# Optimization experiments

Measured on AMD Instinct MI355X. Metric: run time of the kernel, lower is better.

The kernel has to match this reference:

```python
import jax, jax.numpy as jnp
import numpy as np

N = 50000      # nodes
E = 800000     # edges
IN = 128       # in_channels
H = 256        # hidden_channels
EMB = 128      # embedding_size
R = 4          # num_relations
HEADS = 2


def setup_inputs() -> dict:
    key = jax.random.key(0)
    ks = jax.random.split(key, 20)
    w = lambda k, shape: jax.random.normal(k, shape, dtype=jnp.float32) * 0.05
    return dict(
        x=jax.random.normal(ks[0], (N, IN), dtype=jnp.float32),
        edge_index=jax.random.randint(ks[1], (2, E), 0, N, dtype=jnp.int32),
        edge_type=jax.random.randint(ks[2], (E,), 0, R, dtype=jnp.int32),
        sage1_Wl=w(ks[3], (IN, H)), sage1_Wr=w(ks[4], (IN, H)), sage1_b=jnp.zeros((H,), jnp.float32),
        sage2_Wl=w(ks[5], (H, H)), sage2_Wr=w(ks[6], (H, H)), sage2_b=jnp.zeros((H,), jnp.float32),
        gat_W=w(ks[7], (H, HEADS * H)), gat_att_src=w(ks[8], (HEADS, H)), gat_att_dst=w(ks[9], (HEADS, H)),
        gat_b=jnp.zeros((H,), jnp.float32),
        rgcn_Wrel=w(ks[10], (R, H, EMB)), rgcn_Wroot=w(ks[11], (H, EMB)), rgcn_b=jnp.zeros((EMB,), jnp.float32),
        fusion_W=w(ks[12], (H + H + EMB, EMB)), fusion_b=jnp.zeros((EMB,), jnp.float32),
    )


def _segmean(msg, seg, num_segments):
    s = jax.ops.segment_sum(msg, seg, num_segments=num_segments)
    c = jax.ops.segment_sum(jnp.ones((seg.shape[0], 1), msg.dtype), seg, num_segments=num_segments)
    return s / jnp.maximum(c, 1.0)


def _sage(x, src, dst, Wl, Wr, b, n):
    # SAGEConv: lin_l(mean_j x_j) + lin_r(x_i)
    agg = _segmean(x[src], dst, n)
    return agg @ Wl + x @ Wr + b


def _gat(x, src, dst, W, a_src, a_dst, b, n):
    # GATConv heads=2, concat=False (head average), add_self_loops=True
    loop = jnp.arange(n, dtype=src.dtype)
    src = jnp.concatenate([src, loop])
    dst = jnp.concatenate([dst, loop])
    h = (x @ W).reshape(n, HEADS, -1)                 # [N, heads, H]
    al_src = (h * a_src).sum(-1)                      # [N, heads]
    al_dst = (h * a_dst).sum(-1)                      # [N, heads]
    e = jax.nn.leaky_relu(al_src[src] + al_dst[dst], 0.2)   # [E', heads]
    m = jax.ops.segment_max(e, dst, num_segments=n)          # stable softmax per dst node
    ex = jnp.exp(e - m[dst])
    den = jax.ops.segment_sum(ex, dst, num_segments=n)
    alpha = ex / jnp.maximum(den[dst], 1e-16)
    out = jax.ops.segment_sum(alpha[:, :, None] * h[src], dst, num_segments=n)  # [N, heads, H]
    return out.mean(axis=1) + b


def _rgcn(x, src, dst, etype, Wrel, Wroot, b, n, r):
    # RGCNConv: sum_r mean_{j in N_r(i)} W_r x_j + W_root x_i + b
    xt = jnp.einsum('nh,rhe->rne', x, Wrel)           # [R, N, EMB]
    m = xt[etype, src]                                # [E, EMB]
    seg = dst * r + etype                             # per (node, relation) segment
    agg = _segmean(m, seg, n * r).reshape(n, r, -1).sum(axis=1)
    return agg + x @ Wroot + b


def reference(x, edge_index, edge_type,
              sage1_Wl, sage1_Wr, sage1_b,
              sage2_Wl, sage2_Wr, sage2_b,
              gat_W, gat_att_src, gat_att_dst, gat_b,
              rgcn_Wrel, rgcn_Wroot, rgcn_b,
              fusion_W, fusion_b):
    src, dst = edge_index[0], edge_index[1]
    n = x.shape[0]
    x1 = jax.nn.relu(_sage(x, src, dst, sage1_Wl, sage1_Wr, sage1_b, n))
    # dropout(p=0.2) is identity in eval mode
    x_sage = jax.nn.relu(_sage(x1, src, dst, sage2_Wl, sage2_Wr, sage2_b, n))
    x_gat = jax.nn.relu(_gat(x_sage, src, dst, gat_W, gat_att_src, gat_att_dst, gat_b, n))
    x_rgcn = _rgcn(x_gat, src, dst, edge_type, rgcn_Wrel, rgcn_Wroot, rgcn_b, n, R)
    x_all = jnp.concatenate([x_sage, x_gat, x_rgcn], axis=1)
    out = x_all @ fusion_W + fusion_b
    norm = jnp.maximum(jnp.linalg.norm(out, axis=1, keepdims=True), 1e-12)
    return out / norm
```

## Files before the change

kernel.cpp:

```cpp
#include <hip/hip_runtime.h>
#include <hip/hip_fp16.h>
#include <math.h>

constexpr int NN   = 50000;
constexpr int NE   = 800000;
constexpr int NREL = 4;
constexpr int NB   = (NN + 255) / 256;

typedef _Float16 half8 __attribute__((ext_vector_type(8)));
typedef __attribute__((ext_vector_type(4))) float floatx4;

__device__ inline unsigned short f16_rne(float x) {
  return __half_as_ushort(__float2half_rn(x));
}
__device__ inline float h2f(unsigned short h) {
  return __half2float(__ushort_as_half(h));
}

__global__ void k_counts(const int* __restrict__ dst, const int* __restrict__ et,
                         int* cntrel) {
  int e = blockIdx.x * blockDim.x + threadIdx.x;
  if (e < NE) {
    int d = dst[e];
    atomicAdd(&cntrel[d * NREL + et[e]], 1);
  }
}

__global__ void k_scan1(const int* __restrict__ cntrel, int* bsum) {
  __shared__ int sm[256];
  int i = blockIdx.x * 256 + threadIdx.x;
  int v = 0;
  if (i < NN) { int4 c = ((const int4*)cntrel)[i]; v = c.x + c.y + c.z + c.w; }
  sm[threadIdx.x] = v;
  __syncthreads();
  for (int s = 128; s; s >>= 1) {
    if (threadIdx.x < s) sm[threadIdx.x] += sm[threadIdx.x + s];
    __syncthreads();
  }
  if (threadIdx.x == 0) bsum[blockIdx.x] = sm[0];
}
__global__ void k_scan2(const int* __restrict__ bsum, int* boff, int* rowptr) {
  if (threadIdx.x == 0 && blockIdx.x == 0) {
    int acc = 0;
    for (int b = 0; b < NB; ++b) { boff[b] = acc; acc += bsum[b]; }
    rowptr[NN] = NE;
  }
}
__global__ void k_scan3(const int* __restrict__ cntrel, const int* __restrict__ boff,
                        int* rowptr) {
  __shared__ int sm[256];
  int i = blockIdx.x * 256 + threadIdx.x;
  int v = 0;
  if (i < NN) { int4 c = ((const int4*)cntrel)[i]; v = c.x + c.y + c.z + c.w; }
  sm[threadIdx.x] = v;
  __syncthreads();
  for (int s = 1; s < 256; s <<= 1) {
    int t = (threadIdx.x >= s) ? sm[threadIdx.x - s] : 0;
    __syncthreads();
    sm[threadIdx.x] += t;
    __syncthreads();
  }
  if (i < NN) rowptr[i] = boff[blockIdx.x] + sm[threadIdx.x] - v;
}

__global__ void k_fill(const int* __restrict__ src, const int* __restrict__ dst,
                       const int* __restrict__ et, const int* __restrict__ rowptr,
                       int* cursor, int* srcs, int* ets) {
  int e = blockIdx.x * blockDim.x + threadIdx.x;
  if (e >= NE) return;
  int d = dst[e];
  int pos = rowptr[d] + atomicAdd(&cursor[d], 1);
  srcs[pos] = src[e];
  ets[pos]  = et[e];
}

#define PK_N 14
__device__ __constant__ const int PK_BASE[PK_N]  = {0,1,2,3,4,4,5,5,5,5,6,7,7,7};
__device__ __constant__ const int PK_EOFF[PK_N]  = {0,0,0,0,0,256,0,32768,65536,98304,0,0,32768,65536};
__device__ __constant__ const int PK_K[PK_N]     = {128,128,256,256,256,256,256,256,256,256,256,256,256,128};
__device__ __constant__ const int PK_LDB[PK_N]   = {256,256,256,256,512,512,128,128,128,128,128,128,128,128};
__device__ __constant__ const int PK_START[PK_N] = {0,4096,8192,16384,24576,32768,40960,45056,49152,53248,57344,61440,65536,69632};
constexpr int PK_TOTAL = 71680;
constexpr int BF_S1WL = 0,     BF_S1WR = 4096,  BF_S2WL = 8192,  BF_S2WR = 16384;
constexpr int BF_GATW0 = 24576, BF_GATW1 = 32768, BF_WREL = 40960, BF_WROOT = 57344;
constexpr int BF_FW0 = 61440,  BF_FW1 = 65536,  BF_FW2 = 69632;

__global__ void k_pack(const float* b0, const float* b1, const float* b2, const float* b3,
                       const float* b4, const float* b5, const float* b6, const float* b7,
                       unsigned short* __restrict__ Bh) {
  int f = blockIdx.x * 256 + threadIdx.x;
  if (f >= PK_TOTAL) return;
  int m = 0;
#pragma unroll
  for (int i = 1; i < PK_N; ++i) if (f >= PK_START[i]) m = i;
  const float* bases[8] = {b0,b1,b2,b3,b4,b5,b6,b7};
  int lf = f - PK_START[m];
  int K = PK_K[m], ldb = PK_LDB[m];
  int Kq16 = K << 1;
  int ntile = lf / Kq16;
  int rem = lf - ntile * Kq16;
  int kq = rem >> 4, c = rem & 15;
  const float* sp = bases[PK_BASE[m]] + PK_EOFF[m] + (size_t)(kq * 8) * ldb + ntile * 16 + c;
#pragma unroll
  for (int j = 0; j < 8; ++j)
    Bh[(size_t)f * 8 + j] = f16_rne(sp[(size_t)j * ldb]);
}

__global__ void k_split(const float* __restrict__ x, unsigned short* __restrict__ xh,
                        long total4) {
  long i = (long)blockIdx.x * blockDim.x + threadIdx.x;
  if (i >= total4) return;
  float4 v = ((const float4*)x)[i];
  ushort4 h;
  h.x = f16_rne(v.x); h.y = f16_rne(v.y);
  h.z = f16_rne(v.z); h.w = f16_rne(v.w);
  ((ushort4*)xh)[i] = h;
}

__global__ void k_mean128p(const unsigned short* __restrict__ ih, const int* __restrict__ rowptr,
                           const int* __restrict__ srcs,
                           unsigned short* __restrict__ oh) {
  int node = blockIdx.x * 4 + (threadIdx.x >> 6);
  int lane = threadIdx.x & 63;
  if (node >= NN) return;
  int p0 = rowptr[node], p1 = rowptr[node + 1];
  float2 acc = make_float2(0.f, 0.f);
  int p = p0;
  for (; p + 4 <= p1; p += 4) {
    int s0 = srcs[p], s1 = srcs[p+1], s2 = srcs[p+2], s3 = srcs[p+3];
    ushort2 v0 = ((const ushort2*)(ih + ((size_t)s0 << 7)))[lane];
    ushort2 v1 = ((const ushort2*)(ih + ((size_t)s1 << 7)))[lane];
    ushort2 v2 = ((const ushort2*)(ih + ((size_t)s2 << 7)))[lane];
    ushort2 v3 = ((const ushort2*)(ih + ((size_t)s3 << 7)))[lane];
    acc.x += (h2f(v0.x) + h2f(v1.x)) + (h2f(v2.x) + h2f(v3.x));
    acc.y += (h2f(v0.y) + h2f(v1.y)) + (h2f(v2.y) + h2f(v3.y));
  }
  for (; p < p1; ++p) {
    int s = srcs[p];
    ushort2 hv = ((const ushort2*)(ih + ((size_t)s << 7)))[lane];
    acc.x += h2f(hv.x); acc.y += h2f(hv.y);
  }
  float inv = (p1 > p0) ? 1.0f / (float)(p1 - p0) : 0.0f;
  ushort2 h;
  h.x = f16_rne(acc.x * inv); h.y = f16_rne(acc.y * inv);
  size_t o = ((size_t)node << 7) + lane * 2;
  *(ushort2*)(oh + o) = h;
}

__global__ void k_mean256p(const unsigned short* __restrict__ ih, const int* __restrict__ rowptr,
                           const int* __restrict__ srcs,
                           unsigned short* __restrict__ oh) {
  int node = blockIdx.x * 4 + (threadIdx.x >> 6);
  int lane = threadIdx.x & 63;
  if (node >= NN) return;
  int p0 = rowptr[node], p1 = rowptr[node + 1];
  float4 acc = make_float4(0.f, 0.f, 0.f, 0.f);
  int p = p0;
  for (; p + 8 <= p1; p += 8) {
    int ss[8]; ushort4 xr[8];
#pragma unroll
    for (int j = 0; j < 8; ++j) ss[j] = srcs[p + j];
#pragma unroll
    for (int j = 0; j < 8; ++j)
      xr[j] = *(const ushort4*)(ih + ((size_t)ss[j] << 8) + lane * 4);
#pragma unroll
    for (int j = 0; j < 8; ++j) {
      acc.x += h2f(xr[j].x); acc.y += h2f(xr[j].y);
      acc.z += h2f(xr[j].z); acc.w += h2f(xr[j].w);
    }
  }
  for (; p < p1; ++p) {
    int s = srcs[p];
    ushort4 hv = *(const ushort4*)(ih + ((size_t)s << 8) + lane * 4);
    acc.x += h2f(hv.x); acc.y += h2f(hv.y);
    acc.z += h2f(hv.z); acc.w += h2f(hv.w);
  }
  float inv = (p1 > p0) ? 1.0f / (float)(p1 - p0) : 0.0f;
  ushort4 h;
  h.x = f16_rne(acc.x * inv); h.y = f16_rne(acc.y * inv);
  h.z = f16_rne(acc.z * inv); h.w = f16_rne(acc.w * inv);
  size_t o = ((size_t)node << 8) + lane * 4;
  *(ushort4*)(oh + o) = h;
}

__global__ __launch_bounds__(256)
void k_gemm_mfma(const unsigned short* __restrict__ Bph,
                 const unsigned short* A0, int lda0, int bf0, int K0,
                 const unsigned short* A1, int lda1, int bf1, int K1,
                 const unsigned short* A2, int lda2, int bf2, int K2,
                 const float* __restrict__ bias, float* Cf, unsigned short* Ch,
                 int M, int Nc, float scale, int do_relu, int xtmode)
{
  __shared__ short Ash[8*64*8], Bsh[8*64*8];
  const int tid  = threadIdx.x;
  const int lane = tid & 63;
  const int wv   = tid >> 6;
  const int wm   = wv >> 1, wn = wv & 1;
  const int nwg = gridDim.x * gridDim.y;
  const int d   = blockIdx.x + gridDim.x * blockIdx.y;
  const int q   = nwg >> 3, r = nwg & 7;
  const int xcd = d & 7, di = d >> 3;
  const int wg  = (xcd < r ? xcd * (q + 1) : r * (q + 1) + (xcd - r) * q) + di;
  const int row0 = (wg / gridDim.x) * 128;
  const int col0 = (wg % gridDim.x) * 128;

  floatx4 acc[4][4];
#pragma unroll
  for (int i = 0; i < 4; ++i)
#pragma unroll
    for (int j = 0; j < 4; ++j) acc[i][j] = 0;

  const int a_m = tid >> 1;
  const int a_h = tid & 1;
  const int b_nt = tid >> 5;
  const int b_rem = (tid << 1) & 63;

  const unsigned short* Aarr[3] = {A0, A1, A2};
  const int ldaArr[3] = {lda0, lda1, lda2};
  const int bfArr[3]  = {bf0, bf1, bf2};
  const int Karr[3]   = {K0, K1, K2};

  for (int p = 0; p < 3; ++p) {
    const int K = Karr[p];
    if (K == 0) continue;
    const int lda = ldaArr[p];
    const bool arow_ok = (row0 + a_m) < M;
    const unsigned short* Ar = Aarr[p] + (size_t)(row0 + a_m) * lda + a_h * 16;
    const int Kq16 = K << 1;
    const int bbase = bfArr[p] + (col0 >> 4) * Kq16 + b_nt * Kq16 + b_rem;

    for (int kt = 0; kt < K; kt += 32) {
      half8 ah0, ah1;
      if (arow_ok) {
        ah0 = *(const half8*)(const void*)(Ar + kt);
        ah1 = *(const half8*)(const void*)(Ar + kt + 8);
      } else {
#pragma unroll
        for (int i = 0; i < 8; ++i) { ah0[i] = (_Float16)0; ah1[i] = (_Float16)0; }
      }
      const size_t boff = (size_t)(bbase + (kt << 1)) * 8;
      half8 bh0 = *(const half8*)(const void*)(Bph + boff);
      half8 bh1 = *(const half8*)(const void*)(Bph + boff + 8);

      __syncthreads();
      {
        int q2 = a_h * 2;
        int i0 = ((a_m >> 4) * 64 + ((a_m & 15) | (q2 << 4))) * 8;
        int i1 = ((a_m >> 4) * 64 + ((a_m & 15) | ((q2 + 1) << 4))) * 8;
        *(half8*)(void*)&Ash[i0] = ah0;  *(half8*)(void*)&Ash[i1] = ah1;
      }
      {
        int f0 = tid * 2;
        *(half8*)(void*)&Bsh[(size_t)f0 * 8] = bh0;
        *(half8*)(void*)&Bsh[(size_t)(f0 + 1) * 8] = bh1;
      }
      __syncthreads();

      half8 afh[4], bfh[4];
#pragma unroll
      for (int mt = 0; mt < 4; ++mt) {
        int idx = ((wm * 4 + mt) * 64 + lane) * 8;
        afh[mt] = *(half8*)(void*)&Ash[idx];
      }
#pragma unroll
      for (int nt = 0; nt < 4; ++nt) {
        int idx = ((wn * 4 + nt) * 64 + lane) * 8;
        bfh[nt] = *(half8*)(void*)&Bsh[idx];
      }
#pragma unroll
      for (int mt = 0; mt < 4; ++mt)
#pragma unroll
        for (int nt = 0; nt < 4; ++nt)
          acc[mt][nt] = __builtin_amdgcn_mfma_f32_16x16x32_f16(afh[mt], bfh[nt], acc[mt][nt], 0, 0, 0);
    }
  }

  const int cl = lane & 15;
  const int rq = lane >> 4;
#pragma unroll
  for (int mt = 0; mt < 4; ++mt)
#pragma unroll
    for (int r2 = 0; r2 < 4; ++r2) {
      int row = row0 + wm * 64 + mt * 16 + rq * 4 + r2;
      if (row < M) {
#pragma unroll
        for (int nt = 0; nt < 4; ++nt) {
          int colx = col0 + wn * 64 + nt * 16 + cl;
          float vraw = acc[mt][nt][r2] * scale;
          if (xtmode == 2) {
            if (colx < 512) {
              size_t o = (size_t)(colx >> 7) * ((size_t)NN * 128) + (size_t)row * 128 + (colx & 127);
              Ch[o] = f16_rne(vraw);
            } else {
              size_t o = (size_t)row * 128 + (colx & 127);
              Cf[o] = vraw + (bias ? bias[colx & 127] : 0.0f);
            }
          } else {
            float v = vraw + (bias ? bias[colx] : 0.0f);
            if (do_relu) v = fmaxf(v, 0.0f);
            size_t o = (size_t)row * Nc + colx;
            if (Cf) Cf[o] = v;
            if (Ch) Ch[o] = f16_rne(v);
          }
        }
      }
    }
}

__global__ void k_wtilde(const float* __restrict__ gatW, const float* __restrict__ att_s,
                         const float* __restrict__ att_d, float* __restrict__ wt) {
  int k = threadIdx.x;
  const float* Wr = gatW + (size_t)k * 512;
  float s0 = 0, s1 = 0, d0 = 0, d1 = 0;
  for (int i = 0; i < 256; ++i) {
    float w0 = Wr[i], w1 = Wr[256 + i];
    s0 += w0 * att_s[i];       s1 += w1 * att_s[256 + i];
    d0 += w0 * att_d[i];       d1 += w1 * att_d[256 + i];
  }
  wt[k] = s0; wt[256 + k] = s1; wt[512 + k] = d0; wt[768 + k] = d1;
}

__global__ void k_al(const unsigned short* __restrict__ xsh_, const float* __restrict__ wt,
                     float* __restrict__ al_s, float* __restrict__ al_d) {
  int node = blockIdx.x * 4 + (threadIdx.x >> 6);
  int lane = threadIdx.x & 63;
  if (node >= NN) return;
  ushort4 hv = *(const ushort4*)(xsh_ + (size_t)node * 256 + lane * 4);
  float4 v = make_float4(h2f(hv.x), h2f(hv.y), h2f(hv.z), h2f(hv.w));
  const float4* w = (const float4*)wt;
  float4 a0 = w[lane], a1 = w[64 + lane], a2 = w[128 + lane], a3 = w[192 + lane];
  float s0 = v.x*a0.x + v.y*a0.y + v.z*a0.z + v.w*a0.w;
  float s1 = v.x*a1.x + v.y*a1.y + v.z*a1.z + v.w*a1.w;
  float s2 = v.x*a2.x + v.y*a2.y + v.z*a2.z + v.w*a2.w;
  float s3 = v.x*a3.x + v.y*a3.y + v.z*a3.z + v.w*a3.w;
  for (int off = 32; off; off >>= 1) {
    s0 += __shfl_down(s0, off); s1 += __shfl_down(s1, off);
    s2 += __shfl_down(s2, off); s3 += __shfl_down(s3, off);
  }
  if (lane == 0) {
    al_s[node*2] = s0; al_s[node*2 + 1] = s1;
    al_d[node*2] = s2; al_d[node*2 + 1] = s3;
  }
}

__device__ inline float lrelu(float v) { return v > 0.f ? v : 0.2f * v; }

__global__ void k_gat_csr(const unsigned short* __restrict__ xsh_,
                          const int* __restrict__ rowptr, const int* __restrict__ srcs,
                          const float* __restrict__ als, const float* __restrict__ ald,
                          float2* __restrict__ es,
                          unsigned short* __restrict__ aggh) {
  int node = blockIdx.x * 4 + (threadIdx.x >> 6);
  int lane = threadIdx.x & 63;
  if (node >= NN) return;
  int p0 = rowptr[node], p1 = rowptr[node + 1];
  float bd0 = ald[node*2], bd1 = ald[node*2 + 1];
  float vs0 = lrelu(als[node*2] + bd0);
  float vs1 = lrelu(als[node*2 + 1] + bd1);

  float t0 = 0.f, t1 = 0.f;
  for (int p = p0 + lane; p < p1; p += 64) {
    int s = srcs[p];
    float2 a = *(const float2*)(als + (size_t)s * 2);
    float e0 = __expf(lrelu(a.x + bd0));
    float e1 = __expf(lrelu(a.y + bd1));
    es[p] = make_float2(e0, e1);
    t0 += e0; t1 += e1;
  }
  for (int off = 32; off; off >>= 1) {
    t0 += __shfl_xor(t0, off);
    t1 += __shfl_xor(t1, off);
  }
  float w0 = __expf(vs0), w1 = __expf(vs1);
  float den0 = t0 + w0, den1 = t1 + w1;
  __threadfence_block();

  ushort4 hv = *(const ushort4*)(xsh_ + (size_t)node * 256 + lane * 4);
  float4 v = make_float4(h2f(hv.x), h2f(hv.y), h2f(hv.z), h2f(hv.w));
  float4 acc0 = make_float4(w0*v.x, w0*v.y, w0*v.z, w0*v.w);
  float4 acc1 = make_float4(w1*v.x, w1*v.y, w1*v.z, w1*v.w);
  int p = p0;
  for (; p + 8 <= p1; p += 8) {
    int ss[8]; float2 ee[8]; ushort4 xr[8];
#pragma unroll
    for (int j = 0; j < 8; ++j) ss[j] = srcs[p + j];
#pragma unroll
    for (int j = 0; j < 8; ++j) ee[j] = es[p + j];
#pragma unroll
    for (int j = 0; j < 8; ++j)
      xr[j] = *(const ushort4*)(xsh_ + (size_t)ss[j] * 256 + lane * 4);
#pragma unroll
    for (int j = 0; j < 8; ++j) {
      float4 xv = make_float4(h2f(xr[j].x), h2f(xr[j].y), h2f(xr[j].z), h2f(xr[j].w));
      acc0.x += ee[j].x*xv.x; acc0.y += ee[j].x*xv.y;
      acc0.z += ee[j].x*xv.z; acc0.w += ee[j].x*xv.w;
      acc1.x += ee[j].y*xv.x; acc1.y += ee[j].y*xv.y;
      acc1.z += ee[j].y*xv.z; acc1.w += ee[j].y*xv.w;
    }
  }
  for (; p < p1; ++p) {
    int s = srcs[p];
    float2 e = es[p];
    ushort4 xh4 = *(const ushort4*)(xsh_ + (size_t)s * 256 + lane * 4);
    float4 xv = make_float4(h2f(xh4.x), h2f(xh4.y), h2f(xh4.z), h2f(xh4.w));
    acc0.x += e.x*xv.x; acc0.y += e.x*xv.y; acc0.z += e.x*xv.z; acc0.w += e.x*xv.w;
    acc1.x += e.y*xv.x; acc1.y += e.y*xv.y; acc1.z += e.y*xv.z; acc1.w += e.y*xv.w;
  }
  float i0 = 1.0f / fmaxf(den0, 1e-16f);
  float i1 = 1.0f / fmaxf(den1, 1e-16f);
  ushort4 h;
  size_t o = (size_t)node * 512 + lane * 4;
  h.x = f16_rne(acc0.x*i0); h.y = f16_rne(acc0.y*i0);
  h.z = f16_rne(acc0.z*i0); h.w = f16_rne(acc0.w*i0);
  *(ushort4*)(aggh + o) = h;
  h.x = f16_rne(acc1.x*i1); h.y = f16_rne(acc1.y*i1);
  h.z = f16_rne(acc1.z*i1); h.w = f16_rne(acc1.w*i1);
  *(ushort4*)(aggh + o + 256) = h;
}

__global__ void k_rgcn_csr(const unsigned short* __restrict__ xth,
                           const int* __restrict__ rowptr, const int* __restrict__ srcs,
                           const int* __restrict__ ets, const int* __restrict__ cntrel,
                           const float* __restrict__ P3f,
                           unsigned short* __restrict__ oh) {
  int node = blockIdx.x * 4 + (threadIdx.x >> 6);
  int lane = threadIdx.x & 63;
  if (node >= NN) return;
  int p0 = rowptr[node], p1 = rowptr[node + 1];
  float inv0, inv1, inv2, inv3;
  {
    int4 c = ((const int4*)cntrel)[node];
    inv0 = c.x ? 1.0f/(float)c.x : 0.0f;  inv1 = c.y ? 1.0f/(float)c.y : 0.0f;
    inv2 = c.z ? 1.0f/(float)c.z : 0.0f;  inv3 = c.w ? 1.0f/(float)c.w : 0.0f;
  }
  float2 acc = ((const float2*)(P3f + ((size_t)node << 7)))[lane];
  int p = p0;
  for (; p + 8 <= p1; p += 8) {
    int ss[8], rr[8]; ushort2 xr[8];
#pragma unroll
    for (int j = 0; j < 8; ++j) { ss[j] = srcs[p + j]; rr[j] = ets[p + j]; }
#pragma unroll
    for (int j = 0; j < 8; ++j)
      xr[j] = *(const ushort2*)(xth + (((size_t)rr[j] * NN + ss[j]) << 7) + lane * 2);
#pragma unroll
    for (int j = 0; j < 8; ++j) {
      float w = (rr[j] == 0) ? inv0 : (rr[j] == 1) ? inv1 : (rr[j] == 2) ? inv2 : inv3;
      acc.x += h2f(xr[j].x) * w;
      acc.y += h2f(xr[j].y) * w;
    }
  }
  for (; p < p1; ++p) {
    int s = srcs[p], r = ets[p];
    ushort2 hv = *(const ushort2*)(xth + (((size_t)r * NN + s) << 7) + lane * 2);
    float w = (r == 0) ? inv0 : (r == 1) ? inv1 : (r == 2) ? inv2 : inv3;
    acc.x += h2f(hv.x) * w;
    acc.y += h2f(hv.y) * w;
  }
  ushort2 h;
  h.x = f16_rne(acc.x); h.y = f16_rne(acc.y);
  size_t o = ((size_t)node << 7) + lane * 2;
  *(ushort2*)(oh + o) = h;
}

__global__ void k_norm(float* __restrict__ out) {
  int gw = (int)(((long)blockIdx.x * blockDim.x + threadIdx.x) >> 6);
  int lane = threadIdx.x & 63;
  if (gw >= NN) return;
  float2* row = (float2*)(out + (size_t)gw * 128);
  float2 v = row[lane];
  float ss = v.x*v.x + v.y*v.y;
  for (int off = 32; off; off >>= 1) ss += __shfl_down(ss, off);
  ss = __shfl(ss, 0);
  float inv = 1.0f / fmaxf(sqrtf(ss), 1e-12f);
  row[lane] = make_float2(v.x*inv, v.y*inv);
}

extern "C" void kernel_launch(void* const* d_in, const int* in_sizes, int n_in,
                              void* d_out, int out_size, void* d_ws, size_t ws_size,
                              hipStream_t stream)
{
  const float* x     = (const float*)d_in[0];
  const int*   ei    = (const int*)d_in[1];
  const int*   etype = (const int*)d_in[2];
  const float* s1Wl  = (const float*)d_in[3];
  const float* s1Wr  = (const float*)d_in[4];
  const float* s1b   = (const float*)d_in[5];
  const float* s2Wl  = (const float*)d_in[6];
  const float* s2Wr  = (const float*)d_in[7];
  const float* s2b   = (const float*)d_in[8];
  const float* gatW  = (const float*)d_in[9];
  const float* att_s = (const float*)d_in[10];
  const float* att_d = (const float*)d_in[11];
  const float* gatb  = (const float*)d_in[12];
  const float* Wrel  = (const float*)d_in[13];
  const float* Wroot = (const float*)d_in[14];
  const float* rgcnb = (const float*)d_in[15];
  const float* fW    = (const float*)d_in[16];
  const float* fb    = (const float*)d_in[17];
  float* out = (float*)d_out;

  const int* src = ei;
  const int* dst = ei + NE;

  char* ws = (char*)d_ws;
  size_t off = 0;
  auto alloc = [&](size_t bytes) -> void* {
    void* p = ws + off;
    off = (off + bytes + 255) & ~(size_t)255;
    return p;
  };
  int*      deg    = (int*)alloc((size_t)NN * 4);
  int*      cntrel = (int*)alloc((size_t)NN * NREL * 4);
  int*      rowptr = (int*)alloc((size_t)(NN + 1) * 4);
  int*      cursor = (int*)alloc((size_t)NN * 4);
  int*      bsum   = (int*)alloc((size_t)NB * 4);
  int*      boff   = (int*)alloc((size_t)NB * 4);
  int*      srcs   = (int*)alloc((size_t)NE * 4);
  int*      ets    = (int*)alloc((size_t)NE * 4);
  float*    al_s   = (float*)alloc((size_t)NN * 2 * 4);
  float*    al_d   = (float*)alloc((size_t)NN * 2 * 4);
  float*    wt     = (float*)alloc((size_t)4 * 256 * 4);
  unsigned short* PBh = (unsigned short*)alloc((size_t)PK_TOTAL * 8 * 2);
  char* SAb = (char*)alloc((size_t)NN * 1024);
  char* SBb = (char*)alloc((size_t)NN * 1024);
  char* SCb = (char*)alloc((size_t)NN * 1024);
  char* SDb = (char*)alloc((size_t)NN * 1024);
  (void)deg; (void)ws_size; (void)in_sizes; (void)n_in; (void)out_size;

  unsigned short* xh  = (unsigned short*)SAb;
  unsigned short* m1h = xh + (size_t)NN * 128;
  unsigned short* aggh = (unsigned short*)SAb;
  float*          P3f  = (float*)SAb;
  unsigned short* p3h  = (unsigned short*)(SAb + (size_t)NN * 512);
  unsigned short* x1h = (unsigned short*)SBb;
  unsigned short* xth = (unsigned short*)SBb;
  unsigned short* m2h = (unsigned short*)SCb;
  float2*         es  = (float2*)SCb;
  unsigned short* xgh = (unsigned short*)SCb;
  unsigned short* xsh = (unsigned short*)SDb;

  const int NODEB = (NN + 3) / 4;
  const int GY = (NN + 127) / 128;

  k_pack<<<(PK_TOTAL + 255) / 256, 256, 0, stream>>>(s1Wl, s1Wr, s2Wl, s2Wr, gatW, Wrel, Wroot, fW, PBh);
  hipMemsetAsync(cntrel, 0, (size_t)NN * NREL * 4, stream);
  hipMemsetAsync(cursor, 0, (size_t)NN * 4, stream);
  k_counts<<<(NE + 255) / 256, 256, 0, stream>>>(dst, etype, cntrel);
  k_scan1<<<NB, 256, 0, stream>>>(cntrel, bsum);
  k_scan2<<<1, 64, 0, stream>>>(bsum, boff, rowptr);
  k_scan3<<<NB, 256, 0, stream>>>(cntrel, boff, rowptr);
  k_fill<<<(NE + 255) / 256, 256, 0, stream>>>(src, dst, etype, rowptr, cursor, srcs, ets);
  k_split<<<((NN * 128 / 4) + 255) / 256, 256, 0, stream>>>(x, xh, (long)NN * 128 / 4);

  k_mean128p<<<NODEB, 256, 0, stream>>>(xh, rowptr, srcs, m1h);
  k_gemm_mfma<<<dim3(2, GY, 1), 256, 0, stream>>>(PBh,
      m1h, 128, BF_S1WL, 128,  xh, 128, BF_S1WR, 128,  nullptr, 0, 0, 0,
      s1b, nullptr, x1h, NN, 256, 1.0f, 1, 0);

  k_mean256p<<<NODEB, 256, 0, stream>>>(x1h, rowptr, srcs, m2h);
  k_gemm_mfma<<<dim3(2, GY, 1), 256, 0, stream>>>(PBh,
      m2h, 256, BF_S2WL, 256,  x1h, 256, BF_S2WR, 256,  nullptr, 0, 0, 0,
      s2b, nullptr, xsh, NN, 256, 1.0f, 1, 0);

  k_wtilde<<<1, 256, 0, stream>>>(gatW, att_s, att_d, wt);
  k_al<<<NODEB, 256, 0, stream>>>(xsh, wt, al_s, al_d);
  k_gat_csr<<<NODEB, 256, 0, stream>>>(xsh, rowptr, srcs, al_s, al_d, es, aggh);
  k_gemm_mfma<<<dim3(2, GY, 1), 256, 0, stream>>>(PBh,
      aggh, 512, BF_GATW0, 256,  aggh + 256, 512, BF_GATW1, 256,  nullptr, 0, 0, 0,
      gatb, nullptr, xgh, NN, 256, 0.5f, 1, 0);

  k_gemm_mfma<<<dim3(5, GY, 1), 256, 0, stream>>>(PBh,
      xgh, 256, BF_WREL, 256,  nullptr, 0, 0, 0,  nullptr, 0, 0, 0,
      rgcnb, P3f, xth, NN, 640, 1.0f, 0, 2);
  k_rgcn_csr<<<NODEB, 256, 0, stream>>>(xth, rowptr, srcs, ets, cntrel, P3f, p3h);

  k_gemm_mfma<<<dim3(1, GY, 1), 256, 0, stream>>>(PBh,
      xsh, 256, BF_FW0, 256,  xgh, 256, BF_FW1, 256,  p3h, 128, BF_FW2, 128,
      fb, out, nullptr, NN, 128, 1.0f, 0, 0);
  k_norm<<<(NN + 3) / 4, 256, 0, stream>>>(out);
}
```

Before: 712.5 us.

## Load MFMA fragments directly from global memory, dropping LDS staging and barriers

The fp16 MFMA GEMM no longer stages A and B tiles through shared memory with two __syncthreads per k-step. Each wave now loads its own A row fragments and pre-packed B fragments straight from global memory into registers, clamping out-of-range rows to the last valid row, and the k-loop is unrolled by 2. This removes LDS traffic and barrier stalls. In exchange, each A/B fragment is fetched by multiple waves (two waves share each A fragment and two each B fragment), so the kernel leans on L1/L2 for reuse and may issue more global loads.

```diff
diff --git a/kernel.cpp b/kernel.cpp
--- a/kernel.cpp
+++ b/kernel.cpp
@@ -191,7 +191,6 @@
                  const float* __restrict__ bias, float* Cf, unsigned short* Ch,
                  int M, int Nc, float scale, int do_relu, int xtmode)
 {
-  __shared__ short Ash[8*64*8], Bsh[8*64*8];
   const int tid  = threadIdx.x;
   const int lane = tid & 63;
   const int wv   = tid >> 6;
@@ -204,16 +203,14 @@
   const int row0 = (wg / gridDim.x) * 128;
   const int col0 = (wg % gridDim.x) * 128;
 
+  const int c15 = lane & 15;
+  const int k8  = (lane >> 4) * 8;
+
   floatx4 acc[4][4];
 #pragma unroll
   for (int i = 0; i < 4; ++i)
 #pragma unroll
     for (int j = 0; j < 4; ++j) acc[i][j] = 0;
-
-  const int a_m = tid >> 1;
-  const int a_h = tid & 1;
-  const int b_nt = tid >> 5;
-  const int b_rem = (tid << 1) & 63;
 
   const unsigned short* Aarr[3] = {A0, A1, A2};
   const int ldaArr[3] = {lda0, lda1, lda2};
@@ -224,54 +221,33 @@
     const int K = Karr[p];
     if (K == 0) continue;
     const int lda = ldaArr[p];
-    const bool arow_ok = (row0 + a_m) < M;
-    const unsigned short* Ar = Aarr[p] + (size_t)(row0 + a_m) * lda + a_h * 16;
     const int Kq16 = K << 1;
-    const int bbase = bfArr[p] + (col0 >> 4) * Kq16 + b_nt * Kq16 + b_rem;
-
+    const unsigned short* Arow[4];
+#pragma unroll
+    for (int mt = 0; mt < 4; ++mt) {
+      int row = row0 + (wm * 4 + mt) * 16 + c15;
+      if (row > M - 1) row = M - 1;
+      Arow[mt] = Aarr[p] + (size_t)row * lda + k8;
+    }
+    const unsigned short* Brow[4];
+#pragma unroll
+    for (int nt = 0; nt < 4; ++nt)
+      Brow[nt] = Bph + (size_t)(bfArr[p] + ((col0 >> 4) + wn * 4 + nt) * Kq16 + lane) * 8;
+
+#pragma unroll 2
     for (int kt = 0; kt < K; kt += 32) {
-      half8 ah0, ah1;
-      if (arow_ok) {
-        ah0 = *(const half8*)(const void*)(Ar + kt);
-        ah1 = *(const half8*)(const void*)(Ar + kt + 8);
-      } else {
-#pragma unroll
-        for (int i = 0; i < 8; ++i) { ah0[i] = (_Float16)0; ah1[i] = (_Float16)0; }
-      }
-      const size_t boff = (size_t)(bbase + (kt << 1)) * 8;
-      half8 bh0 = *(const half8*)(const void*)(Bph + boff);
-      half8 bh1 = *(const half8*)(const void*)(Bph + boff + 8);
-
-      __syncthreads();
-      {
-        int q2 = a_h * 2;
-        int i0 = ((a_m >> 4) * 64 + ((a_m & 15) | (q2 << 4))) * 8;
-        int i1 = ((a_m >> 4) * 64 + ((a_m & 15) | ((q2 + 1) << 4))) * 8;
-        *(half8*)(void*)&Ash[i0] = ah0;  *(half8*)(void*)&Ash[i1] = ah1;
-      }
-      {
-        int f0 = tid * 2;
-        *(half8*)(void*)&Bsh[(size_t)f0 * 8] = bh0;
-        *(half8*)(void*)&Bsh[(size_t)(f0 + 1) * 8] = bh1;
-      }
-      __syncthreads();
-
-      half8 afh[4], bfh[4];
-#pragma unroll
-      for (int mt = 0; mt < 4; ++mt) {
-        int idx = ((wm * 4 + mt) * 64 + lane) * 8;
-        afh[mt] = *(half8*)(void*)&Ash[idx];
-      }
-#pragma unroll
-      for (int nt = 0; nt < 4; ++nt) {
-        int idx = ((wn * 4 + nt) * 64 + lane) * 8;
-        bfh[nt] = *(half8*)(void*)&Bsh[idx];
-      }
+      half8 af[4], bfq[4];
 #pragma unroll
       for (int mt = 0; mt < 4; ++mt)
+        af[mt] = *(const half8*)(const void*)(Arow[mt] + kt);
+#pragma unroll
+      for (int nt = 0; nt < 4; ++nt)
+        bfq[nt] = *(const half8*)(const void*)(Brow[nt] + (size_t)(kt << 1) * 8);
+#pragma unroll
+      for (int mt = 0; mt < 4; ++mt)
 #pragma unroll
         for (int nt = 0; nt < 4; ++nt)
-          acc[mt][nt] = __builtin_amdgcn_mfma_f32_16x16x32_f16(afh[mt], bfh[nt], acc[mt][nt], 0, 0, 0);
+          acc[mt][nt] = __builtin_amdgcn_mfma_f32_16x16x32_f16(af[mt], bfq[nt], acc[mt][nt], 0, 0, 0);
     }
   }
 
```

Result: slower. 762.0 us (+7.0%).
